# Kernel optimization log

Hardware: AMD Instinct MI355X
Metric: run time of the kernel (lower is better)

The kernel has to match this reference:

```python
import jax, jax.numpy as jnp
import numpy as np

MIN_NORM = 1e-15
EPS = 1e-7
N_NODES = 100000
N_EDGES = 1600000
D_IN = 256
D_OUT = 128

# ---- Hyperboloid manifold ops (HGCN-style) ----

def proj_tan0(u, c):
    # zero out the time (first) coordinate
    return jnp.concatenate([jnp.zeros_like(u[..., :1]), u[..., 1:]], axis=-1)

def proj(x, c):
    # project onto hyperboloid: recompute time coord from space coords
    K = 1.0 / c
    y = x[..., 1:]
    t = jnp.sqrt(jnp.clip(K + jnp.sum(y * y, axis=-1, keepdims=True), EPS, None))
    return jnp.concatenate([t, y], axis=-1)

def expmap0(u, c):
    sqrtK = jnp.sqrt(1.0 / c)
    x = u[..., 1:]
    nrm = jnp.clip(jnp.linalg.norm(x, axis=-1, keepdims=True), MIN_NORM, None)
    theta = nrm / sqrtK
    t0 = sqrtK * jnp.cosh(theta)
    rest = sqrtK * jnp.sinh(theta) * x / nrm
    return proj(jnp.concatenate([t0, rest], axis=-1), c)

def logmap0(x, c):
    sqrtK = jnp.sqrt(1.0 / c)
    y = x[..., 1:]
    nrm = jnp.clip(jnp.linalg.norm(y, axis=-1, keepdims=True), MIN_NORM, None)
    theta = jnp.clip(x[..., :1] / sqrtK, 1.0 + EPS, None)
    rest = sqrtK * jnp.arccosh(theta) * y / nrm
    return jnp.concatenate([jnp.zeros_like(rest[..., :1]), rest], axis=-1)

def mobius_matvec1(m, x, c):
    # weight is (in, out): map via tangent space at origin
    return expmap0(logmap0(x, c) @ m, c)

def mobius_matvec0(n, x, c):
    # per-node scalar (N,1) scaling in tangent space
    return expmap0(n * logmap0(x, c), c)

def mobius_add(x, y, c):
    # tangent-space addition at origin (broadcasts over bias rows)
    return expmap0(logmap0(x, c) + logmap0(y, c), c)

mobius_add0 = mobius_add

def spmm(rows, cols, vals, x):
    # COO sparse adj @ dense x  ->  [N, d]
    return jax.ops.segment_sum(vals[:, None] * x[cols], rows, num_segments=N_NODES)

def gcn_layer(x, weight, bias, rows, cols, vals, c):
    out = mobius_matvec1(weight, x, c)
    hyp_bias = proj(expmap0(proj_tan0(bias[None, :], c), c), c)
    out = mobius_add(out, hyp_bias, c)
    out = logmap0(out, c)
    out = spmm(rows, cols, vals, out)
    return proj(expmap0(out, c), c)


def setup_inputs() -> dict:
    key = jax.random.key(0)
    ks = jax.random.split(key, 12)
    A1_tensor = jax.random.normal(ks[0], (N_NODES, D_IN), dtype=jnp.float32)
    adj_rows = jax.random.randint(ks[1], (N_EDGES,), 0, N_NODES)
    adj_cols = jax.random.randint(ks[2], (N_EDGES,), 0, N_NODES)
    adj_vals = jax.random.uniform(ks[3], (N_EDGES,), dtype=jnp.float32) / 16.0
    raw_c = jnp.full((1,), np.log(np.e - 1.0), dtype=jnp.float32)
    bnd_in = 1.0 / np.sqrt(D_IN)
    bnd_h = 1.0 / np.sqrt(D_OUT)
    Lin1 = jax.random.uniform(ks[4], (D_IN, D_OUT), jnp.float32, -bnd_in, bnd_in)
    Lin1_bias = jax.random.uniform(ks[5], (D_OUT,), jnp.float32, -bnd_in, bnd_in)
    n = jax.random.uniform(ks[6], (N_NODES, 1), jnp.float32, 0.0, 1.0)
    gc1_weight = jax.random.uniform(ks[7], (D_IN, D_OUT), jnp.float32, -bnd_in, bnd_in)
    gc1_bias = jax.random.uniform(ks[8], (D_OUT,), jnp.float32, -bnd_in, bnd_in)
    gc2_weight = jax.random.uniform(ks[9], (D_OUT, D_OUT), jnp.float32, -bnd_h, bnd_h)
    gc2_bias = jax.random.uniform(ks[10], (D_OUT,), jnp.float32, -bnd_h, bnd_h)
    return {"A1_tensor": A1_tensor, "adj_rows": adj_rows, "adj_cols": adj_cols,
            "adj_vals": adj_vals, "raw_c": raw_c, "Lin1": Lin1, "Lin1_bias": Lin1_bias,
            "n": n, "gc1_weight": gc1_weight, "gc1_bias": gc1_bias,
            "gc2_weight": gc2_weight, "gc2_bias": gc2_bias}


def reference(A1_tensor, adj_rows, adj_cols, adj_vals, raw_c, Lin1, Lin1_bias, n,
              gc1_weight, gc1_bias, gc2_weight, gc2_bias):
    c = jax.nn.softplus(raw_c) + 1e-5  # learned curvature, shape (1,)
    # dropout is identity at inference
    x_tan = proj_tan0(A1_tensor, c)
    a = proj(expmap0(x_tan, c), c)
    # skip branch: hyperbolic linear
    a1 = mobius_matvec1(Lin1, a, c)
    hyp_bias = proj(expmap0(proj_tan0(Lin1_bias[None, :], c), c), c)
    a1 = mobius_add(a1, hyp_bias, c)
    a2 = mobius_matvec0(n, a1, c)
    # GCN layer 1 + gated residual
    x_1 = gcn_layer(a, gc1_weight, gc1_bias, adj_rows, adj_cols, adj_vals, c)
    x_1 = mobius_matvec0(1.0 - n, x_1, c)
    x_1 = mobius_add0(x_1, a2, c)
    # GCN layer 2
    x_2 = gcn_layer(x_1, gc2_weight, gc2_bias, adj_rows, adj_cols, adj_vals, c)
    x_2 = logmap0(x_2, c)
    x_2 = jnp.concatenate([x_2, a1], axis=-1)  # [N, 2*D_OUT]
    x_2 = expmap0(x_2, c)
    return (x_2, c)
```

## Files before the change

### kernel.cpp

```cpp
#include <hip/hip_runtime.h>
#include <math.h>


#define NN 100000
#define MAXDEG 64
#define NB 391
#define CAP 5120
#define EPT 16
#define EPB 4096

typedef __attribute__((ext_vector_type(8))) short bf16x8;
typedef __attribute__((ext_vector_type(4))) float f32x4;

__device__ __forceinline__ float wsum(float v) {
#pragma unroll
  for (int off = 32; off > 0; off >>= 1) v += __shfl_xor(v, off, 64);
  return v;
}

__device__ __forceinline__ float sane(float v) {
  return fminf(fmaxf(v, -3.0e38f), 3.0e38f);
}

__device__ __forceinline__ float b2f(ushort h) {
  union { unsigned u; float f; } z; z.u = (unsigned)h << 16; return z.f;
}
__device__ __forceinline__ ushort f2b(float f) {
  union { float f; unsigned u; } z; z.f = f;
  unsigned u = z.u;
  unsigned r = (u + 0x7fffu + ((u >> 16) & 1u)) >> 16;
  return (ushort)r;
}

__global__ void setup_kernel(const float* __restrict__ raw_c, float* __restrict__ SC) {
  float rc = raw_c[0];
  float c = fmaxf(rc, 0.0f) + log1pf(expf(-fabsf(rc))) + 1e-5f;
  SC[0] = c;
  SC[1] = 1.0f / c;
  SC[2] = sqrtf(1.0f / c);
}

__global__ __launch_bounds__(256) void convA_kernel(const float* __restrict__ A1,
                                                    ushort* __restrict__ A1h) {
  long i = (long)blockIdx.x * 256 + threadIdx.x;
  const long total = (long)NN * 256 / 8;
  if (i >= total) return;
  const float* p = A1 + i * 8;
  float4 v0 = *(const float4*)p;
  float4 v1 = *(const float4*)(p + 4);
  ushort t[8] = {f2b(v0.x), f2b(v0.y), f2b(v0.z), f2b(v0.w),
                 f2b(v1.x), f2b(v1.y), f2b(v1.z), f2b(v1.w)};
  if (((i * 8) & 255) == 0) t[0] = 0;
  *(uint4*)(A1h + i * 8) = *(uint4*)t;
}

__global__ void wconv_kernel(const float* __restrict__ W, ushort* __restrict__ Bt, int K) {
  int i = blockIdx.x * 256 + threadIdx.x;
  if (i < K * 128) {
    int k = i >> 7, n = i & 127;
    Bt[(size_t)n * K + k] = f2b(W[i]);
  }
}

__global__ __launch_bounds__(256) void mfma_gemm_kernel(const ushort* __restrict__ A, int lda,
                                                        const ushort* __restrict__ Bt,
                                                        ushort* __restrict__ C,
                                                        const float* __restrict__ bias,
                                                        int M, int K) {
  __shared__ ushort As[128][40];
  __shared__ ushort Bs[128][40];
  const int tid = threadIdx.x;
  const int w = tid >> 6, l = tid & 63;
  const int wr = w >> 1, wc = w & 1;
  const int lane16 = l & 15, quad = l >> 4;
  const int bm = blockIdx.x * 128;
  f32x4 acc[4][4];
#pragma unroll
  for (int mt = 0; mt < 4; ++mt)
#pragma unroll
    for (int nt = 0; nt < 4; ++nt) acc[mt][nt] = (f32x4){0.f, 0.f, 0.f, 0.f};

  for (int k0 = 0; k0 < K; k0 += 32) {
#pragma unroll
    for (int p = 0; p < 2; ++p) {
      int idx = p * 256 + tid;
      int row = idx >> 2;
      int kc = (idx & 3) * 8;
      int grow = bm + row;
      uint4 av = make_uint4(0, 0, 0, 0);
      if (grow < M) av = *(const uint4*)(A + (size_t)grow * lda + k0 + kc);
      *(uint4*)(&As[row][kc]) = av;
      uint4 bv = *(const uint4*)(Bt + (size_t)row * K + k0 + kc);
      *(uint4*)(&Bs[row][kc]) = bv;
    }
    __syncthreads();
    bf16x8 af[4], bfr[4];
#pragma unroll
    for (int mt = 0; mt < 4; ++mt)
      af[mt] = *(const bf16x8*)(&As[wr * 64 + mt * 16 + lane16][quad * 8]);
#pragma unroll
    for (int nt = 0; nt < 4; ++nt)
      bfr[nt] = *(const bf16x8*)(&Bs[wc * 64 + nt * 16 + lane16][quad * 8]);
#pragma unroll
    for (int mt = 0; mt < 4; ++mt)
#pragma unroll
      for (int nt = 0; nt < 4; ++nt)
        acc[mt][nt] = __builtin_amdgcn_mfma_f32_16x16x32_bf16(af[mt], bfr[nt], acc[mt][nt], 0, 0, 0);
    __syncthreads();
  }
#pragma unroll
  for (int mt = 0; mt < 4; ++mt) {
#pragma unroll
    for (int r = 0; r < 4; ++r) {
      int row = bm + wr * 64 + mt * 16 + quad * 4 + r;
      if (row < M) {
#pragma unroll
        for (int nt = 0; nt < 4; ++nt) {
          int col = wc * 64 + nt * 16 + lane16;
          float v = acc[mt][nt][r] + ((col == 0) ? 0.0f : bias[col]);
          C[(size_t)row * 128 + col] = f2b(v);
        }
      }
    }
  }
}

__global__ void zero_int_kernel(int* __restrict__ p, int n) {
  int i = blockIdx.x * blockDim.x + threadIdx.x;
  if (i < n) p[i] = 0;
}

__global__ __launch_bounds__(256) void part1_kernel(const int* __restrict__ rows,
                                                    const int* __restrict__ cols,
                                                    const float* __restrict__ vals,
                                                    int* __restrict__ bucketCnt,
                                                    uint2* __restrict__ store, int E) {
  __shared__ int hist[NB];
  __shared__ int cursor[NB];
  const int tid = threadIdx.x;
  for (int t = tid; t < NB; t += 256) hist[t] = 0;
  __syncthreads();
  const long base = (long)blockIdx.x * EPB;
  int rw[EPT];
  unsigned pk[EPT];
#pragma unroll
  for (int k = 0; k < EPT; ++k) {
    long i = base + (long)k * 256 + tid;
    rw[k] = -1;
    if (i < E) {
      rw[k] = rows[i];
      pk[k] = ((unsigned)cols[i] << 15) | ((unsigned)f2b(vals[i]) & 0x7FFFu);
      atomicAdd(&hist[rw[k] >> 8], 1);
    }
  }
  __syncthreads();
  for (int t = tid; t < NB; t += 256) {
    int h = hist[t];
    cursor[t] = (h > 0) ? atomicAdd(&bucketCnt[t], h) : 0;
  }
  __syncthreads();
#pragma unroll
  for (int k = 0; k < EPT; ++k) {
    if (rw[k] >= 0) {
      int b = rw[k] >> 8;
      int pos = atomicAdd(&cursor[b], 1);
      if (pos < CAP) store[(size_t)b * CAP + pos] = make_uint2(pk[k], (unsigned)rw[k]);
    }
  }
}

__global__ __launch_bounds__(256) void part2_kernel(const int* __restrict__ bucketCnt,
                                                    const uint2* __restrict__ store,
                                                    int* __restrict__ deg,
                                                    unsigned* __restrict__ eCV) {
  __shared__ int d2[256];
  const int b = blockIdx.x, tid = threadIdx.x;
  d2[tid] = 0;
  __syncthreads();
  int n = bucketCnt[b];
  n = (n > CAP) ? CAP : n;
  const uint2* bs = store + (size_t)b * CAP;
  for (int i = tid; i < n; i += 256) {
    uint2 rec = bs[i];
    int rl = rec.y & 255;
    int k = atomicAdd(&d2[rl], 1);
    if (k < MAXDEG) eCV[((size_t)rec.y << 6) + k] = rec.x;
  }
  __syncthreads();
  int gr = b * 256 + tid;
  if (gr < NN) deg[gr] = d2[tid];
}

template <int Q>
__device__ __forceinline__ void gather_batch(const ushort* __restrict__ Gh,
                                             unsigned mine, int j, int lo,
                                             float& a0, float& a1) {
  unsigned pj[Q];
  ushort2 u[Q];
#pragma unroll
  for (int q = 0; q < Q; ++q) {
    pj[q] = (unsigned)__builtin_amdgcn_readlane((int)mine, j + q);
    u[q] = *(const ushort2*)(Gh + ((size_t)(pj[q] >> 15) << 7) + lo);
  }
#pragma unroll
  for (int q = 0; q < Q; ++q) {
    union { unsigned u32; float f; } vv; vv.u32 = (pj[q] & 0x7FFFu) << 16;
    a0 = fmaf(vv.f, b2f(u[q].x), a0);
    a1 = fmaf(vv.f, b2f(u[q].y), a1);
  }
}

__device__ __forceinline__ void row_gather(int row, int l,
                                           const int* __restrict__ deg,
                                           const unsigned* __restrict__ eCV,
                                           const ushort* __restrict__ Gh,
                                           float& a0, float& a1) {
  unsigned mine = eCV[(size_t)row * MAXDEG + l];
  int dg = __builtin_amdgcn_readfirstlane(deg[row]);
  dg = (dg > MAXDEG) ? MAXDEG : dg;
  a0 = 0.0f; a1 = 0.0f;
  const int lo = l << 1;
  int j = 0;
  for (; j + 16 <= dg; j += 16) gather_batch<16>(Gh, mine, j, lo, a0, a1);
  if (j + 8 <= dg) { gather_batch<8>(Gh, mine, j, lo, a0, a1); j += 8; }
  if (j + 4 <= dg) { gather_batch<4>(Gh, mine, j, lo, a0, a1); j += 4; }
  for (; j < dg; ++j) gather_batch<1>(Gh, mine, j, lo, a0, a1);
}

__global__ __launch_bounds__(256) void spmm1_kernel(const int* __restrict__ deg,
                                                    const unsigned* __restrict__ eCV,
                                                    const ushort* __restrict__ G1h,
                                                    const ushort* __restrict__ Pb,
                                                    const float* __restrict__ nvec,
                                                    const float* __restrict__ SC,
                                                    ushort* __restrict__ TBh,
                                                    float* __restrict__ A1P) {
  int row = __builtin_amdgcn_readfirstlane(blockIdx.x * 4 + (threadIdx.x >> 6));
  int l = threadIdx.x & 63;
  if (row >= NN) return;
  float sK = SC[2];
  float nval = nvec[row];
  float a0, a1;
  row_gather(row, l, deg, eCV, G1h, a0, a1);
  ushort2 pu = *(const ushort2*)(Pb + (size_t)row * 128 + 2 * l);
  float p0 = b2f(pu.x), p1 = b2f(pu.y);
  float t10 = (l == 0) ? 0.0f : fmaf(1.0f - nval, a0, nval * p0);
  float t11 = fmaf(1.0f - nval, a1, nval * p1);
  ushort2 tb; tb.x = f2b(t10); tb.y = f2b(t11);
  *(ushort2*)(TBh + (size_t)row * 128 + 2 * l) = tb;
  float px = (l == 0) ? 0.0f : p0;
  float py = p1;
  float ss = wsum(px * px + py * py);
  float nrm = fmaxf(sqrtf(ss), 1e-15f);
  float th = nrm / sK;
  float sc = sK * sinhf(th) / nrm;
  float t = sK * coshf(th);
  float2 st;
  st.x = (l == 0) ? t : sc * px;
  st.y = sc * py;
  *(float2*)(A1P + (size_t)row * 128 + 2 * l) = st;
}

__global__ __launch_bounds__(256) void spmm2_kernel(const int* __restrict__ deg,
                                                    const unsigned* __restrict__ eCV,
                                                    const ushort* __restrict__ G2h,
                                                    const float* __restrict__ A1P,
                                                    const float* __restrict__ SC,
                                                    float* __restrict__ out) {
  int row = __builtin_amdgcn_readfirstlane(blockIdx.x * 4 + (threadIdx.x >> 6));
  int l = threadIdx.x & 63;
  if (row >= NN) return;
  float cval = SC[0], K = SC[1], sK = SC[2];
  float a0, a1;
  row_gather(row, l, deg, eCV, G2h, a0, a1);
  float u0 = (l == 0) ? 0.0f : a0;
  float u1 = a1;
  float2 ap = *(const float2*)(A1P + (size_t)row * 128 + 2 * l);
  float u2 = ap.x, u3 = ap.y;
  float ss = wsum(u0 * u0 + u1 * u1 + u2 * u2 + u3 * u3);
  float nrm = fmaxf(sqrtf(ss), 1e-15f);
  float th = nrm / sK;
  float sc = sK * sinhf(th) / nrm;
  float o0 = sc * u0, o1 = sc * u1, o2 = sc * u2, o3 = sc * u3;
  if (l == 0) o0 = 0.0f;
  float sy = wsum(o0 * o0 + o1 * o1 + o2 * o2 + o3 * o3);
  float t2 = sqrtf(fmaxf(K + sy, 1e-7f));
  float* op = out + (size_t)row * 256;
  float2 w0, w1;
  w0.x = sane((l == 0) ? t2 : o0);
  w0.y = sane(o1);
  w1.x = sane(o2);
  w1.y = sane(o3);
  *(float2*)(op + 2 * l) = w0;
  *(float2*)(op + 128 + 2 * l) = w1;
  if (row == 0 && l == 0) out[(size_t)NN * 256] = cval;
}

extern "C" void kernel_launch(void* const* d_in, const int* in_sizes, int n_in,
                              void* d_out, int out_size, void* d_ws, size_t ws_size,
                              hipStream_t stream) {
  const float* A1  = (const float*)d_in[0];
  const int* rows  = (const int*)d_in[1];
  const int* cols  = (const int*)d_in[2];
  const float* vals = (const float*)d_in[3];
  const float* rawc = (const float*)d_in[4];
  const float* Lin1 = (const float*)d_in[5];
  const float* Lb   = (const float*)d_in[6];
  const float* nv   = (const float*)d_in[7];
  const float* g1w  = (const float*)d_in[8];
  const float* g1b  = (const float*)d_in[9];
  const float* g2w  = (const float*)d_in[10];
  const float* g2b  = (const float*)d_in[11];
  float* out = (float*)d_out;
  float* ws = (float*)d_ws;
  const int E = in_sizes[1];

  float*  SC   = ws;
  ushort* A1h  = (ushort*)(ws + 256);
  ushort* Pb   = A1h + (size_t)256 * NN;
  ushort* G1h  = Pb + (size_t)128 * NN;
  ushort* TBh  = G1h + (size_t)128 * NN;
  float*  A1P  = (float*)(TBh + (size_t)128 * NN);
  ushort* Bt1  = (ushort*)(A1P + (size_t)128 * NN);
  ushort* Btg1 = Bt1 + 128 * 256;
  ushort* Btg2 = Btg1 + 128 * 256;
  int* deg      = (int*)(Btg2 + 128 * 256);
  unsigned* eCV = (unsigned*)(deg + 100096);
  uint2* store   = (uint2*)A1P;
  int* bucketCnt = (int*)(store + (size_t)NB * CAP);

  const int rowBlocks = (NN + 3) / 4;
  const int gemmGrid = (NN + 127) / 128;
  const int p1Blocks = (E + EPB - 1) / EPB;

  zero_int_kernel<<<2, 256, 0, stream>>>(bucketCnt, NB);
  part1_kernel<<<p1Blocks, 256, 0, stream>>>(rows, cols, vals, bucketCnt, store, E);
  part2_kernel<<<NB, 256, 0, stream>>>(bucketCnt, store, deg, eCV);

  setup_kernel<<<1, 1, 0, stream>>>(rawc, SC);
  convA_kernel<<<(NN * 256 / 8 + 255) / 256, 256, 0, stream>>>(A1, A1h);
  wconv_kernel<<<(256 * 128 + 255) / 256, 256, 0, stream>>>(Lin1, Bt1, 256);
  wconv_kernel<<<(256 * 128 + 255) / 256, 256, 0, stream>>>(g1w, Btg1, 256);
  wconv_kernel<<<(128 * 128 + 255) / 256, 256, 0, stream>>>(g2w, Btg2, 128);
  mfma_gemm_kernel<<<gemmGrid, 256, 0, stream>>>(A1h, 256, Bt1, Pb, Lb, NN, 256);
  mfma_gemm_kernel<<<gemmGrid, 256, 0, stream>>>(A1h, 256, Btg1, G1h, g1b, NN, 256);
  spmm1_kernel<<<rowBlocks, 256, 0, stream>>>(deg, eCV, G1h, Pb, nv, SC, TBh, A1P);
  mfma_gemm_kernel<<<gemmGrid, 256, 0, stream>>>(TBh, 128, Btg2, G1h, g2b, NN, 128);
  spmm2_kernel<<<rowBlocks, 256, 0, stream>>>(deg, eCV, G1h, A1P, SC, out);
}
```

Baseline: 491.5 us.

## Merge prep kernels, store A1P in bf16, simplify gather loop and fast hyperbolic math

Five small setup launches (zeroing bucket counts, curvature setup, three weight conversions) are folded into one prep kernel to cut launch overhead. The intermediate A1P is stored as bf16 instead of fp32, halving its write and read traffic between the two SpMM kernels. The gather loop is unified into fixed 16-wide batches with clamped indices and masked weights, and sinh/cosh/sqrt are replaced with exp/rsq/rcp intrinsics plus an algebraic shortcut that drops the second wave reduction. These trade some precision and redundant tail loads for fewer instructions and less memory traffic.

```diff
diff --git a/kernel.cpp b/kernel.cpp
--- a/kernel.cpp
+++ b/kernel.cpp
@@ -32,12 +32,35 @@
   return (ushort)r;
 }
 
-__global__ void setup_kernel(const float* __restrict__ raw_c, float* __restrict__ SC) {
-  float rc = raw_c[0];
-  float c = fmaxf(rc, 0.0f) + log1pf(expf(-fabsf(rc))) + 1e-5f;
-  SC[0] = c;
-  SC[1] = 1.0f / c;
-  SC[2] = sqrtf(1.0f / c);
+__global__ __launch_bounds__(256) void prep_kernel(const float* __restrict__ Lin1,
+                                                   const float* __restrict__ g1w,
+                                                   const float* __restrict__ g2w,
+                                                   ushort* __restrict__ Bt1,
+                                                   ushort* __restrict__ Btg1,
+                                                   ushort* __restrict__ Btg2,
+                                                   int* __restrict__ bucketCnt,
+                                                   const float* __restrict__ raw_c,
+                                                   float* __restrict__ SC) {
+  int i = blockIdx.x * 256 + threadIdx.x;
+  if (i < 32768) {
+    int k = i >> 7, n = i & 127;
+    Bt1[n * 256 + k] = f2b(Lin1[i]);
+  } else if (i < 65536) {
+    int j = i - 32768, k = j >> 7, n = j & 127;
+    Btg1[n * 256 + k] = f2b(g1w[j]);
+  } else if (i < 81920) {
+    int j = i - 65536, k = j >> 7, n = j & 127;
+    Btg2[n * 128 + k] = f2b(g2w[j]);
+  } else if (i < 81920 + NB) {
+    bucketCnt[i - 81920] = 0;
+  } else if (i == 81920 + NB) {
+    float rc = raw_c[0];
+    float c = fmaxf(rc, 0.0f) + log1pf(expf(-fabsf(rc))) + 1e-5f;
+    SC[0] = c;
+    SC[1] = 1.0f / c;
+    SC[2] = sqrtf(1.0f / c);
+    SC[3] = sqrtf(c);
+  }
 }
 
 __global__ __launch_bounds__(256) void convA_kernel(const float* __restrict__ A1,
@@ -52,14 +75,6 @@
                  f2b(v1.x), f2b(v1.y), f2b(v1.z), f2b(v1.w)};
   if (((i * 8) & 255) == 0) t[0] = 0;
   *(uint4*)(A1h + i * 8) = *(uint4*)t;
-}
-
-__global__ void wconv_kernel(const float* __restrict__ W, ushort* __restrict__ Bt, int K) {
-  int i = blockIdx.x * 256 + threadIdx.x;
-  if (i < K * 128) {
-    int k = i >> 7, n = i & 127;
-    Bt[(size_t)n * K + k] = f2b(W[i]);
-  }
 }
 
 __global__ __launch_bounds__(256) void mfma_gemm_kernel(const ushort* __restrict__ A, int lda,
@@ -125,11 +140,6 @@
   }
 }
 
-__global__ void zero_int_kernel(int* __restrict__ p, int n) {
-  int i = blockIdx.x * blockDim.x + threadIdx.x;
-  if (i < n) p[i] = 0;
-}
-
 __global__ __launch_bounds__(256) void part1_kernel(const int* __restrict__ rows,
                                                     const int* __restrict__ cols,
                                                     const float* __restrict__ vals,
@@ -189,25 +199,6 @@
   __syncthreads();
   int gr = b * 256 + tid;
   if (gr < NN) deg[gr] = d2[tid];
-}
-
-template <int Q>
-__device__ __forceinline__ void gather_batch(const ushort* __restrict__ Gh,
-                                             unsigned mine, int j, int lo,
-                                             float& a0, float& a1) {
-  unsigned pj[Q];
-  ushort2 u[Q];
-#pragma unroll
-  for (int q = 0; q < Q; ++q) {
-    pj[q] = (unsigned)__builtin_amdgcn_readlane((int)mine, j + q);
-    u[q] = *(const ushort2*)(Gh + ((size_t)(pj[q] >> 15) << 7) + lo);
-  }
-#pragma unroll
-  for (int q = 0; q < Q; ++q) {
-    union { unsigned u32; float f; } vv; vv.u32 = (pj[q] & 0x7FFFu) << 16;
-    a0 = fmaf(vv.f, b2f(u[q].x), a0);
-    a1 = fmaf(vv.f, b2f(u[q].y), a1);
-  }
 }
 
 __device__ __forceinline__ void row_gather(int row, int l,
@@ -220,11 +211,24 @@
   dg = (dg > MAXDEG) ? MAXDEG : dg;
   a0 = 0.0f; a1 = 0.0f;
   const int lo = l << 1;
-  int j = 0;
-  for (; j + 16 <= dg; j += 16) gather_batch<16>(Gh, mine, j, lo, a0, a1);
-  if (j + 8 <= dg) { gather_batch<8>(Gh, mine, j, lo, a0, a1); j += 8; }
-  if (j + 4 <= dg) { gather_batch<4>(Gh, mine, j, lo, a0, a1); j += 4; }
-  for (; j < dg; ++j) gather_batch<1>(Gh, mine, j, lo, a0, a1);
+  for (int j = 0; j < dg; j += 16) {
+    unsigned pj[16];
+    ushort2 u[16];
+#pragma unroll
+    for (int q = 0; q < 16; ++q) {
+      int kk = j + q;
+      kk = (kk < dg) ? kk : (dg - 1);
+      pj[q] = (unsigned)__builtin_amdgcn_readlane((int)mine, kk);
+      u[q] = *(const ushort2*)(Gh + ((size_t)(pj[q] >> 15) << 7) + lo);
+    }
+#pragma unroll
+    for (int q = 0; q < 16; ++q) {
+      union { unsigned u32; float f; } vv;
+      vv.u32 = (j + q < dg) ? ((pj[q] & 0x7FFFu) << 16) : 0u;
+      a0 = fmaf(vv.f, b2f(u[q].x), a0);
+      a1 = fmaf(vv.f, b2f(u[q].y), a1);
+    }
+  }
 }
 
 __global__ __launch_bounds__(256) void spmm1_kernel(const int* __restrict__ deg,
@@ -234,11 +238,11 @@
                                                     const float* __restrict__ nvec,
                                                     const float* __restrict__ SC,
                                                     ushort* __restrict__ TBh,
-                                                    float* __restrict__ A1P) {
+                                                    ushort* __restrict__ A1Ph) {
   int row = __builtin_amdgcn_readfirstlane(blockIdx.x * 4 + (threadIdx.x >> 6));
   int l = threadIdx.x & 63;
   if (row >= NN) return;
-  float sK = SC[2];
+  float sK = SC[2], rsK = SC[3];
   float nval = nvec[row];
   float a0, a1;
   row_gather(row, l, deg, eCV, G1h, a0, a1);
@@ -251,40 +255,46 @@
   float px = (l == 0) ? 0.0f : p0;
   float py = p1;
   float ss = wsum(px * px + py * py);
-  float nrm = fmaxf(sqrtf(ss), 1e-15f);
-  float th = nrm / sK;
-  float sc = sK * sinhf(th) / nrm;
-  float t = sK * coshf(th);
-  float2 st;
-  st.x = (l == 0) ? t : sc * px;
-  st.y = sc * py;
-  *(float2*)(A1P + (size_t)row * 128 + 2 * l) = st;
+  float rinv = fminf(__builtin_amdgcn_rsqf(ss), 1e15f);
+  float nrm = ss * rinv;
+  float th = nrm * rsK;
+  float e = __expf(th);
+  float ei = __builtin_amdgcn_rcpf(e);
+  float sh = 0.5f * (e - ei), ch = 0.5f * (e + ei);
+  float sc = sK * sh * rinv;
+  float t = sK * ch;
+  ushort2 st;
+  st.x = f2b((l == 0) ? t : sc * px);
+  st.y = f2b(sc * py);
+  *(ushort2*)(A1Ph + (size_t)row * 128 + 2 * l) = st;
 }
 
 __global__ __launch_bounds__(256) void spmm2_kernel(const int* __restrict__ deg,
                                                     const unsigned* __restrict__ eCV,
                                                     const ushort* __restrict__ G2h,
-                                                    const float* __restrict__ A1P,
+                                                    const ushort* __restrict__ A1Ph,
                                                     const float* __restrict__ SC,
                                                     float* __restrict__ out) {
   int row = __builtin_amdgcn_readfirstlane(blockIdx.x * 4 + (threadIdx.x >> 6));
   int l = threadIdx.x & 63;
   if (row >= NN) return;
-  float cval = SC[0], K = SC[1], sK = SC[2];
+  float cval = SC[0], K = SC[1], sK = SC[2], rsK = SC[3];
   float a0, a1;
   row_gather(row, l, deg, eCV, G2h, a0, a1);
   float u0 = (l == 0) ? 0.0f : a0;
   float u1 = a1;
-  float2 ap = *(const float2*)(A1P + (size_t)row * 128 + 2 * l);
-  float u2 = ap.x, u3 = ap.y;
+  ushort2 ap = *(const ushort2*)(A1Ph + (size_t)row * 128 + 2 * l);
+  float u2 = b2f(ap.x), u3 = b2f(ap.y);
   float ss = wsum(u0 * u0 + u1 * u1 + u2 * u2 + u3 * u3);
-  float nrm = fmaxf(sqrtf(ss), 1e-15f);
-  float th = nrm / sK;
-  float sc = sK * sinhf(th) / nrm;
+  float rinv = fminf(__builtin_amdgcn_rsqf(ss), 1e15f);
+  float nrm = ss * rinv;
+  float th = nrm * rsK;
+  float e = __expf(th);
+  float ei = __builtin_amdgcn_rcpf(e);
+  float sc = sK * (0.5f * (e - ei)) * rinv;
   float o0 = sc * u0, o1 = sc * u1, o2 = sc * u2, o3 = sc * u3;
   if (l == 0) o0 = 0.0f;
-  float sy = wsum(o0 * o0 + o1 * o1 + o2 * o2 + o3 * o3);
-  float t2 = sqrtf(fmaxf(K + sy, 1e-7f));
+  float t2 = sqrtf(fmaxf(K + sc * sc * ss, 1e-7f));
   float* op = out + (size_t)row * 256;
   float2 w0, w1;
   w0.x = sane((l == 0) ? t2 : o0);
@@ -320,31 +330,29 @@
   ushort* Pb   = A1h + (size_t)256 * NN;
   ushort* G1h  = Pb + (size_t)128 * NN;
   ushort* TBh  = G1h + (size_t)128 * NN;
-  float*  A1P  = (float*)(TBh + (size_t)128 * NN);
-  ushort* Bt1  = (ushort*)(A1P + (size_t)128 * NN);
+  ushort* A1Ph = TBh + (size_t)128 * NN;
+  ushort* Bt1  = A1Ph + (size_t)128 * NN;
   ushort* Btg1 = Bt1 + 128 * 256;
   ushort* Btg2 = Btg1 + 128 * 256;
   int* deg      = (int*)(Btg2 + 128 * 256);
   unsigned* eCV = (unsigned*)(deg + 100096);
-  uint2* store   = (uint2*)A1P;
+  uint2* store   = (uint2*)A1Ph;
   int* bucketCnt = (int*)(store + (size_t)NB * CAP);
 
   const int rowBlocks = (NN + 3) / 4;
   const int gemmGrid = (NN + 127) / 128;
   const int p1Blocks = (E + EPB - 1) / EPB;
-
-  zero_int_kernel<<<2, 256, 0, stream>>>(bucketCnt, NB);
+  const int prepBlocks = (81920 + NB + 1 + 255) / 256;
+
+  prep_kernel<<<prepBlocks, 256, 0, stream>>>(Lin1, g1w, g2w, Bt1, Btg1, Btg2,
+                                              bucketCnt, rawc, SC);
   part1_kernel<<<p1Blocks, 256, 0, stream>>>(rows, cols, vals, bucketCnt, store, E);
   part2_kernel<<<NB, 256, 0, stream>>>(bucketCnt, store, deg, eCV);
 
-  setup_kernel<<<1, 1, 0, stream>>>(rawc, SC);
   convA_kernel<<<(NN * 256 / 8 + 255) / 256, 256, 0, stream>>>(A1, A1h);
-  wconv_kernel<<<(256 * 128 + 255) / 256, 256, 0, stream>>>(Lin1, Bt1, 256);
-  wconv_kernel<<<(256 * 128 + 255) / 256, 256, 0, stream>>>(g1w, Btg1, 256);
-  wconv_kernel<<<(128 * 128 + 255) / 256, 256, 0, stream>>>(g2w, Btg2, 128);
   mfma_gemm_kernel<<<gemmGrid, 256, 0, stream>>>(A1h, 256, Bt1, Pb, Lb, NN, 256);
   mfma_gemm_kernel<<<gemmGrid, 256, 0, stream>>>(A1h, 256, Btg1, G1h, g1b, NN, 256);
-  spmm1_kernel<<<rowBlocks, 256, 0, stream>>>(deg, eCV, G1h, Pb, nv, SC, TBh, A1P);
+  spmm1_kernel<<<rowBlocks, 256, 0, stream>>>(deg, eCV, G1h, Pb, nv, SC, TBh, A1Ph);
   mfma_gemm_kernel<<<gemmGrid, 256, 0, stream>>>(TBh, 128, Btg2, G1h, g2b, NN, 128);
-  spmm2_kernel<<<rowBlocks, 256, 0, stream>>>(deg, eCV, G1h, A1P, SC, out);
-}
+  spmm2_kernel<<<rowBlocks, 256, 0, stream>>>(deg, eCV, G1h, A1Ph, SC, out);
+}
```

Result: faster. 462.5 us (-5.9%).
